# Optimization experiments

Hardware: AMD Instinct MI355X
Metric: run time of the kernel (lower is better)

Reference implementation:

```python
import jax, jax.numpy as jnp
import numpy as np

N_HEADS = 16

def setup_inputs() -> dict:
    key = jax.random.key(0)
    ks = jax.random.split(key, 8)
    B, S, D = 2, 2048, 1024
    s = 0.02
    return {
        "hidden_states": jax.random.normal(ks[0], (B, S, D), jnp.float32),
        "attention_mask": jnp.ones((B, S), jnp.int32),
        "script_types": jax.random.randint(ks[1], (B, S), 0, 4),
        "Wq": jax.random.normal(ks[2], (D, D), jnp.float32) * s,
        "bq": jnp.zeros((D,), jnp.float32),
        "Wk": jax.random.normal(ks[3], (D, D), jnp.float32) * s,
        "bk": jnp.zeros((D,), jnp.float32),
        "Wv": jax.random.normal(ks[4], (D, D), jnp.float32) * s,
        "bv": jnp.zeros((D,), jnp.float32),
        "Wo": jax.random.normal(ks[5], (D, D), jnp.float32) * s,
        "bo": jnp.zeros((D,), jnp.float32),
        "script_w": jnp.ones((4, N_HEADS), jnp.float32),
    }

def _heads(x, H):
    B, S, D = x.shape
    return x.reshape(B, S, H, D // H).transpose(0, 2, 1, 3)  # [B,H,S,hd]

def reference(hidden_states, attention_mask, script_types, Wq, bq, Wk, bk, Wv, bv, Wo, bo, script_w):
    B, S, D = hidden_states.shape
    H = N_HEADS
    hd = D // H
    q = _heads(hidden_states @ Wq + bq, H)
    k = _heads(hidden_states @ Wk + bk, H)
    v = _heads(hidden_states @ Wv + bv, H)
    # script-dependent per-head query scaling: [B,S,H] -> [B,H,S,1]
    sw = script_w[script_types].transpose(0, 2, 1)[..., None]
    q = q * sw
    scores = jnp.einsum("bhqd,bhkd->bhqk", q, k) / jnp.sqrt(jnp.float32(hd))
    mask = attention_mask[:, None, None, :]  # [B,1,1,S]
    scores = jnp.where(mask == 0, -jnp.inf, scores)
    probs = jax.nn.softmax(scores, axis=-1)  # dropout is identity in eval mode
    ctx = jnp.einsum("bhqk,bhkd->bhqd", probs, v)
    ctx = ctx.transpose(0, 2, 1, 3).reshape(B, S, D)
    out = ctx @ Wo + bo
    return out, probs
```

## Files before the change

kernel.cpp:

```cpp
#include <hip/hip_runtime.h>
#include <hip/hip_bf16.h>
#include <cstdint>
#include <cstddef>

typedef __attribute__((ext_vector_type(8))) short short8;
typedef __attribute__((ext_vector_type(4))) float f32x4;

#define MFMA16(a,b,c) __builtin_amdgcn_mfma_f32_16x16x32_bf16((a),(b),(c),0,0,0)
#define NEG_INF (-__builtin_inff())

__device__ __forceinline__ unsigned short f2bf(float f) {
    union { float f; unsigned int u; } a; a.f = f;
    return (unsigned short)((a.u + 0x7FFFu + ((a.u >> 16) & 1u)) >> 16);
}

__device__ __forceinline__ void gload16(const void* g, void* l) {
    __builtin_amdgcn_global_load_lds(
        (const __attribute__((address_space(1))) void*)g,
        (__attribute__((address_space(3))) void*)l, 16, 0, 0);
}

__global__ __launch_bounds__(256) void prep(const float* __restrict__ X,
                                            unsigned short* __restrict__ Xb,
                                            const float* __restrict__ Wq,
                                            const float* __restrict__ Wk,
                                            const float* __restrict__ Wv,
                                            const float* __restrict__ Wo,
                                            unsigned short* __restrict__ WqkvT,
                                            unsigned short* __restrict__ WoT,
                                            const float* __restrict__ bq,
                                            const float* __restrict__ bk,
                                            const float* __restrict__ bv,
                                            float* __restrict__ biasq) {
    const int bid = blockIdx.x;
    const int t = threadIdx.x;
    if (bid < 4096) {
        int i = (bid * 256 + t) * 4;
        float4 v = *(const float4*)(X + i);
        ushort4 o;
        o.x = f2bf(v.x); o.y = f2bf(v.y); o.z = f2bf(v.z); o.w = f2bf(v.w);
        *(ushort4*)(Xb + i) = o;
    } else if (bid < 8192) {
        __shared__ float tile[32][33];
        const int wid = bid - 4096;
        const int which = wid >> 10, t32 = wid & 1023;
        const float* W = (which == 0) ? Wq : (which == 1) ? Wk : (which == 2) ? Wv : Wo;
        unsigned short* WT = (which < 3) ? (WqkvT + which * 1048576) : WoT;
        int tx = t & 31, ty = t >> 5;
        int kb = (t32 & 31) * 32, nb = (t32 >> 5) * 32;
        #pragma unroll
        for (int r = 0; r < 32; r += 8)
            tile[ty + r][tx] = W[(size_t)(kb + ty + r) * 1024 + nb + tx];
        __syncthreads();
        #pragma unroll
        for (int r = 0; r < 32; r += 8) {
            float v = tile[tx][ty + r];
            WT[(size_t)(nb + ty + r) * 1024 + kb + tx] = f2bf(v);
        }
    } else {
        for (int i = t; i < 3072; i += 256) {
            const float* s = (i < 1024) ? bq : (i < 2048) ? bk : bv;
            biasq[i] = s[i & 1023];
        }
    }
}

__global__ __launch_bounds__(256) void gemm_qkv(const unsigned short* __restrict__ A,
                                                const unsigned short* __restrict__ BT,
                                                const float* __restrict__ bias,
                                                unsigned short* __restrict__ qk_out,
                                                unsigned short* __restrict__ vt_out) {
    __shared__ alignas(16) unsigned short As[4096];
    __shared__ alignas(16) unsigned short Bs[4096];
    const int t = threadIdx.x;
    const int wave = t >> 6, lane = t & 63, quad = lane >> 4, l16 = lane & 15;
    const int m0 = blockIdx.x * 128, n0 = blockIdx.y * 128;
    const int wm = (wave >> 1) * 64, wn = (wave & 1) * 64;
    const int r4 = lane >> 2, c16 = (lane & 3) << 4;
    const char* Ag = (const char*)A + (size_t)(m0 + wave * 32 + r4) * 2048 + c16;
    const char* Bg = (const char*)BT + (size_t)(n0 + wave * 32 + r4) * 2048 + c16;
    char* Al = (char*)As + wave * 2048;
    char* Bl = (char*)Bs + wave * 2048;
    f32x4 acc[4][4] = {};
    for (int k0 = 0; k0 < 1024; k0 += 32) {
        __syncthreads();
        gload16(Ag + k0 * 2, Al);
        gload16(Ag + k0 * 2 + 32768, Al + 1024);
        gload16(Bg + k0 * 2, Bl);
        gload16(Bg + k0 * 2 + 32768, Bl + 1024);
        __syncthreads();
        short8 af[4], bfr[4];
        #pragma unroll
        for (int i = 0; i < 4; i++)
            af[i] = *(const short8*)((const char*)As + (wm + i * 16 + l16) * 64 + (quad << 4));
        #pragma unroll
        for (int j = 0; j < 4; j++)
            bfr[j] = *(const short8*)((const char*)Bs + (wn + j * 16 + l16) * 64 + (quad << 4));
        #pragma unroll
        for (int i = 0; i < 4; i++)
            #pragma unroll
            for (int j = 0; j < 4; j++)
                acc[i][j] = MFMA16(af[i], bfr[j], acc[i][j]);
    }
    #pragma unroll
    for (int i = 0; i < 4; i++) {
        int tokb = m0 + wm + i * 16 + quad * 4;
        int b = tokb >> 11, s = tokb & 2047;
        #pragma unroll
        for (int j = 0; j < 4; j++) {
            int n = n0 + wn + j * 16 + l16;
            float bv = bias[n];
            int which = n >> 10, n1 = n & 1023, h = n1 >> 6, d = n1 & 63;
            if (which == 2) {
                ushort4 pv;
                pv.x = f2bf(acc[i][j][0] + bv);
                pv.y = f2bf(acc[i][j][1] + bv);
                pv.z = f2bf(acc[i][j][2] + bv);
                pv.w = f2bf(acc[i][j][3] + bv);
                *(ushort4*)(vt_out + ((size_t)(b * 16 + h) * 64 + d) * 2048 + s) = pv;
            } else {
                #pragma unroll
                for (int r = 0; r < 4; r++) {
                    float v = acc[i][j][r] + bv;
                    qk_out[(size_t)which * 4194304 +
                           (((size_t)(b * 16 + h)) * 2048 + s + r) * 64 + d] = f2bf(v);
                }
            }
        }
    }
}

__global__ __launch_bounds__(256) void gemm_out(const unsigned short* __restrict__ A,
                                                const unsigned short* __restrict__ BT,
                                                const float* __restrict__ bias,
                                                float* __restrict__ C) {
    __shared__ alignas(16) unsigned short As[2048];
    __shared__ alignas(16) unsigned short Bs[4096];
    const int t = threadIdx.x;
    const int wave = t >> 6, lane = t & 63, quad = lane >> 4, l16 = lane & 15;
    const int m0 = blockIdx.x * 64, n0 = blockIdx.y * 128;
    const int wm = (wave >> 1) * 32, wn = (wave & 1) * 64;
    const int r4 = lane >> 2, c16 = (lane & 3) << 4;
    const char* Ag = (const char*)A + (size_t)(m0 + wave * 16 + r4) * 2048 + c16;
    const char* Bg = (const char*)BT + (size_t)(n0 + wave * 32 + r4) * 2048 + c16;
    char* Al = (char*)As + wave * 1024;
    char* Bl = (char*)Bs + wave * 2048;
    f32x4 acc[2][4] = {};
    for (int k0 = 0; k0 < 1024; k0 += 32) {
        __syncthreads();
        gload16(Ag + k0 * 2, Al);
        gload16(Bg + k0 * 2, Bl);
        gload16(Bg + k0 * 2 + 32768, Bl + 1024);
        __syncthreads();
        short8 af[2], bfr[4];
        #pragma unroll
        for (int i = 0; i < 2; i++)
            af[i] = *(const short8*)((const char*)As + (wm + i * 16 + l16) * 64 + (quad << 4));
        #pragma unroll
        for (int j = 0; j < 4; j++)
            bfr[j] = *(const short8*)((const char*)Bs + (wn + j * 16 + l16) * 64 + (quad << 4));
        #pragma unroll
        for (int i = 0; i < 2; i++)
            #pragma unroll
            for (int j = 0; j < 4; j++)
                acc[i][j] = MFMA16(af[i], bfr[j], acc[i][j]);
    }
    #pragma unroll
    for (int i = 0; i < 2; i++) {
        int tokb = m0 + wm + i * 16 + quad * 4;
        #pragma unroll
        for (int j = 0; j < 4; j++) {
            int n = n0 + wn + j * 16 + l16;
            float bv = bias[n];
            #pragma unroll
            for (int r = 0; r < 4; r++)
                C[(size_t)(tokb + r) * 1024 + n] = acc[i][j][r] + bv;
        }
    }
}

__global__ __launch_bounds__(512, 4) void attn(const unsigned short* __restrict__ Q,
                                               const unsigned short* __restrict__ K,
                                               const unsigned short* __restrict__ Vt,
                                               const int* __restrict__ amask,
                                               const int* __restrict__ stypes,
                                               const float* __restrict__ script_w,
                                               float* __restrict__ probs,
                                               unsigned short* __restrict__ ctx) {
    __shared__ alignas(16) unsigned short Ks[2][4096];
    __shared__ alignas(16) unsigned short Vts[2][4096];
    __shared__ alignas(16) unsigned short Ps[8][16][64];
    const int t = threadIdx.x;
    const int wave = t >> 6, lane = t & 63, quad = lane >> 4, l16 = lane & 15;
    const int bid = blockIdx.y * 16 + blockIdx.x;
    const int swz = (bid & 7) * 64 + (bid >> 3);
    const int qt = swz & 15, bh = swz >> 4;
    const int b = bh >> 4, h = bh & 15;
    const int q0 = qt * 128;
    const int qrow = q0 + wave * 16 + l16;
    const int sx16 = (l16 & 7) << 4;

    const int st = stypes[b * 2048 + qrow];
    const float sfac = script_w[st * 16 + h] * 0.125f;

    const size_t qbase = ((size_t)bh * 2048 + qrow) * 64;
    const short8 aQ0 = *(const short8*)(Q + qbase + quad * 8);
    const short8 aQ1 = *(const short8*)(Q + qbase + 32 + quad * 8);

    const char* Kg = (const char*)(K + (size_t)bh * 131072);
    const char* Vg = (const char*)(Vt + (size_t)bh * 131072);
    const int* am = amask + b * 2048;

    const int r8 = lane >> 3;
    const int cx = ((lane & 7) ^ r8) << 4;

#define STAGE_K(kt_, buf_) \
    gload16(Kg + (size_t)(kt_) * 8192 + (wave * 8 + r8) * 128 + cx, \
            (char*)&Ks[buf_][0] + wave * 1024)
#define STAGE_V(kt_, buf_) \
    gload16(Vg + (size_t)(wave * 8 + r8) * 4096 + (kt_) * 128 + cx, \
            (char*)&Vts[buf_][0] + wave * 1024)

    float lsum = 0.f;
    STAGE_K(0, 0);
    __syncthreads();
    {
        int cur = 0;
        for (int kt = 0; kt < 32; kt++) {
            if (kt < 31) STAGE_K(kt + 1, cur ^ 1);
            __builtin_amdgcn_sched_barrier(0);
            f32x4 sc[4] = {};
            const char* kbl = (const char*)&Ks[cur][0];
            __builtin_amdgcn_s_setprio(1);
            #pragma unroll
            for (int j = 0; j < 4; j++) {
                const char* rp = kbl + (j * 16 + l16) * 128;
                short8 bk0 = *(const short8*)(rp + ((quad << 4) ^ sx16));
                short8 bk1 = *(const short8*)(rp + ((64 + (quad << 4)) ^ sx16));
                sc[j] = MFMA16(bk0, aQ0, sc[j]);
                sc[j] = MFMA16(bk1, aQ1, sc[j]);
            }
            __builtin_amdgcn_s_setprio(0);
            #pragma unroll
            for (int j = 0; j < 4; j++) {
                int4 mi = *(const int4*)(am + kt * 64 + j * 16 + quad * 4);
                lsum += __expf(fmaf(sc[j][0], sfac, mi.x ? 0.f : NEG_INF));
                lsum += __expf(fmaf(sc[j][1], sfac, mi.y ? 0.f : NEG_INF));
                lsum += __expf(fmaf(sc[j][2], sfac, mi.z ? 0.f : NEG_INF));
                lsum += __expf(fmaf(sc[j][3], sfac, mi.w ? 0.f : NEG_INF));
            }
            __syncthreads();
            cur ^= 1;
        }
    }
    lsum += __shfl_xor(lsum, 16, 64);
    lsum += __shfl_xor(lsum, 32, 64);
    const float lbias = (lsum > 0.f) ? -__logf(lsum) : NEG_INF;

    f32x4 oacc[4] = {};
    STAGE_K(0, 0);
    STAGE_V(0, 0);
    asm volatile("s_waitcnt vmcnt(0)" ::: "memory");
    __builtin_amdgcn_s_barrier();
    __builtin_amdgcn_sched_barrier(0);
    {
        int cur = 0;
        char* psrow = (char*)&Ps[wave][l16][0];
        for (int kt = 0; kt < 32; kt++) {
            if (kt < 31) { STAGE_K(kt + 1, cur ^ 1); STAGE_V(kt + 1, cur ^ 1); }
            __builtin_amdgcn_sched_barrier(0);
            f32x4 sc[4] = {};
            const char* kbl = (const char*)&Ks[cur][0];
            __builtin_amdgcn_s_setprio(1);
            #pragma unroll
            for (int j = 0; j < 4; j++) {
                const char* rp = kbl + (j * 16 + l16) * 128;
                short8 bk0 = *(const short8*)(rp + ((quad << 4) ^ sx16));
                short8 bk1 = *(const short8*)(rp + ((64 + (quad << 4)) ^ sx16));
                sc[j] = MFMA16(bk0, aQ0, sc[j]);
                sc[j] = MFMA16(bk1, aQ1, sc[j]);
            }
            __builtin_amdgcn_s_setprio(0);
            short8 v0[4], v1[4];
            const char* vbl = (const char*)&Vts[cur][0];
            #pragma unroll
            for (int j2 = 0; j2 < 4; j2++) {
                const char* rp = vbl + (j2 * 16 + l16) * 128;
                v0[j2] = *(const short8*)(rp + ((quad << 4) ^ sx16));
                v1[j2] = *(const short8*)(rp + ((64 + (quad << 4)) ^ sx16));
            }
            const size_t pbase = ((size_t)bh * 2048 + qrow) * 2048 + kt * 64 + quad * 4;
            #pragma unroll
            for (int j = 0; j < 4; j++) {
                int4 mi = *(const int4*)(am + kt * 64 + j * 16 + quad * 4);
                float p0 = __expf(fmaf(sc[j][0], sfac, mi.x ? lbias : NEG_INF));
                float p1 = __expf(fmaf(sc[j][1], sfac, mi.y ? lbias : NEG_INF));
                float p2 = __expf(fmaf(sc[j][2], sfac, mi.z ? lbias : NEG_INF));
                float p3 = __expf(fmaf(sc[j][3], sfac, mi.w ? lbias : NEG_INF));
                f32x4 pv; pv[0] = p0; pv[1] = p1; pv[2] = p2; pv[3] = p3;
                __builtin_nontemporal_store(pv, (f32x4*)(probs + pbase + j * 16));
                ushort4 pq; pq.x = f2bf(p0); pq.y = f2bf(p1); pq.z = f2bf(p2); pq.w = f2bf(p3);
                *(ushort4*)(psrow + ((j * 32 + quad * 8) ^ sx16)) = pq;
            }
            asm volatile("s_waitcnt lgkmcnt(0)" ::: "memory");
            __builtin_amdgcn_sched_barrier(0);
            short8 aP0 = *(const short8*)(psrow + ((quad << 4) ^ sx16));
            short8 aP1 = *(const short8*)(psrow + ((64 + (quad << 4)) ^ sx16));
            __builtin_amdgcn_s_setprio(1);
            #pragma unroll
            for (int j2 = 0; j2 < 4; j2++) oacc[j2] = MFMA16(aP0, v0[j2], oacc[j2]);
            #pragma unroll
            for (int j2 = 0; j2 < 4; j2++) oacc[j2] = MFMA16(aP1, v1[j2], oacc[j2]);
            __builtin_amdgcn_s_setprio(0);
            asm volatile("s_waitcnt vmcnt(4)" ::: "memory");
            __builtin_amdgcn_s_barrier();
            __builtin_amdgcn_sched_barrier(0);
            cur ^= 1;
        }
    }
#undef STAGE_K
#undef STAGE_V
    #pragma unroll
    for (int j2 = 0; j2 < 4; j2++)
        #pragma unroll
        for (int r = 0; r < 4; r++) {
            int qr = q0 + wave * 16 + quad * 4 + r;
            ctx[((size_t)b * 2048 + qr) * 1024 + h * 64 + j2 * 16 + l16] = f2bf(oacc[j2][r]);
        }
}

extern "C" void kernel_launch(void* const* d_in, const int* in_sizes, int n_in,
                              void* d_out, int out_size, void* d_ws, size_t ws_size,
                              hipStream_t stream) {
    const float* X    = (const float*)d_in[0];
    const int*  amask = (const int*)d_in[1];
    const int*  stp   = (const int*)d_in[2];
    const float* Wq   = (const float*)d_in[3];
    const float* bq   = (const float*)d_in[4];
    const float* Wk   = (const float*)d_in[5];
    const float* bk   = (const float*)d_in[6];
    const float* Wv   = (const float*)d_in[7];
    const float* bv   = (const float*)d_in[8];
    const float* Wo   = (const float*)d_in[9];
    const float* bo   = (const float*)d_in[10];
    const float* sw   = (const float*)d_in[11];

    float* out   = (float*)d_out;
    float* probs = out + 4194304;

    char* ws = (char*)d_ws;
    unsigned short* Xb    = (unsigned short*)(ws);
    unsigned short* WqkvT = (unsigned short*)(ws + 8388608);
    unsigned short* WoT   = (unsigned short*)(ws + 14680064);
    float*          biasq = (float*)(ws + 16777216);
    unsigned short* Qb    = (unsigned short*)(ws + 16789504);
    unsigned short* Vtb   = (unsigned short*)(ws + 41955328);
    unsigned short* Ctx   = (unsigned short*)(ws + 50343936);
    unsigned short* Kb    = Qb + 4194304;

    prep<<<8193, 256, 0, stream>>>(X, Xb, Wq, Wk, Wv, Wo, WqkvT, WoT, bq, bk, bv, biasq);
    gemm_qkv<<<dim3(32, 24), 256, 0, stream>>>(Xb, WqkvT, biasq, Qb, Vtb);
    attn<<<dim3(16, 32), 512, 0, stream>>>(Qb, Kb, Vtb, amask, stp, sw, probs, Ctx);
    gemm_out<<<dim3(64, 8), 256, 0, stream>>>(Ctx, WoT, bo, out);
}
```

Baseline: 296.7 us.

## Triple-buffer K/V tiles and software-pipeline QK^T of the next tile in attention

Expands the K and V LDS staging from double to triple buffers, prefetching two tiles ahead. It also computes the next tile's QK^T scores while the current tile's softmax and PV work runs, to overlap MFMA with the exp and store work. The attention mask is converted once into an additive float bias in LDS. The softmax now multiplies by a reciprocal sum instead of adding a log bias, and uses packed v_cvt_pk_bf16 conversion. V fragments are loaded in two halves to cut register pressure. The larger LDS footprint (about 72KB per block) may reduce the number of resident blocks per CU, and vmcnt(4) now also waits on the two-ahead prefetch.

```diff
diff --git a/kernel.cpp b/kernel.cpp
--- a/kernel.cpp
+++ b/kernel.cpp
@@ -12,6 +12,12 @@
 __device__ __forceinline__ unsigned short f2bf(float f) {
     union { float f; unsigned int u; } a; a.f = f;
     return (unsigned short)((a.u + 0x7FFFu + ((a.u >> 16) & 1u)) >> 16);
+}
+
+__device__ __forceinline__ unsigned int cvtpk_bf16(float a, float b) {
+    unsigned int r;
+    asm("v_cvt_pk_bf16_f32 %0, %1, %2" : "=v"(r) : "v"(a), "v"(b));
+    return r;
 }
 
 __device__ __forceinline__ void gload16(const void* g, void* l) {
@@ -187,9 +193,10 @@
                                                const float* __restrict__ script_w,
                                                float* __restrict__ probs,
                                                unsigned short* __restrict__ ctx) {
-    __shared__ alignas(16) unsigned short Ks[2][4096];
-    __shared__ alignas(16) unsigned short Vts[2][4096];
+    __shared__ alignas(16) unsigned short KsA[3][4096];
+    __shared__ alignas(16) unsigned short VtsA[3][4096];
     __shared__ alignas(16) unsigned short Ps[8][16][64];
+    __shared__ alignas(16) float mb[2048];
     const int t = threadIdx.x;
     const int wave = t >> 6, lane = t & 63, quad = lane >> 4, l16 = lane & 15;
     const int bid = blockIdx.y * 16 + blockIdx.x;
@@ -209,117 +216,121 @@
 
     const char* Kg = (const char*)(K + (size_t)bh * 131072);
     const char* Vg = (const char*)(Vt + (size_t)bh * 131072);
-    const int* am = amask + b * 2048;
+
+    {
+        int4 m4 = *(const int4*)(amask + b * 2048 + t * 4);
+        f32x4 mv;
+        mv[0] = m4.x ? 0.f : NEG_INF;
+        mv[1] = m4.y ? 0.f : NEG_INF;
+        mv[2] = m4.z ? 0.f : NEG_INF;
+        mv[3] = m4.w ? 0.f : NEG_INF;
+        *(f32x4*)&mb[t * 4] = mv;
+    }
 
     const int r8 = lane >> 3;
     const int cx = ((lane & 7) ^ r8) << 4;
-
-#define STAGE_K(kt_, buf_) \
-    gload16(Kg + (size_t)(kt_) * 8192 + (wave * 8 + r8) * 128 + cx, \
-            (char*)&Ks[buf_][0] + wave * 1024)
-#define STAGE_V(kt_, buf_) \
-    gload16(Vg + (size_t)(wave * 8 + r8) * 4096 + (kt_) * 128 + cx, \
-            (char*)&Vts[buf_][0] + wave * 1024)
+    char* KsB = (char*)&KsA[0][0];
+    char* VtsB = (char*)&VtsA[0][0];
+
+#define STAGE_K(kt_, ob_) \
+    gload16(Kg + (size_t)(kt_) * 8192 + (wave * 8 + r8) * 128 + cx, KsB + (ob_) + wave * 1024)
+#define STAGE_V(kt_, ob_) \
+    gload16(Vg + (size_t)(wave * 8 + r8) * 4096 + (kt_) * 128 + cx, VtsB + (ob_) + wave * 1024)
+#define QKT(dst_, ob_) do { \
+        const char* _kb = KsB + (ob_); \
+        _Pragma("unroll") \
+        for (int _j = 0; _j < 4; _j++) { \
+            const char* _rp = _kb + (_j * 16 + l16) * 128; \
+            short8 _k0 = *(const short8*)(_rp + ((quad << 4) ^ sx16)); \
+            short8 _k1 = *(const short8*)(_rp + ((64 + (quad << 4)) ^ sx16)); \
+            dst_[_j] = MFMA16(_k0, aQ0, dst_[_j]); \
+            dst_[_j] = MFMA16(_k1, aQ1, dst_[_j]); \
+        } } while (0)
+
+    int ob0 = 0, ob1 = 8192, ob2 = 16384;
 
     float lsum = 0.f;
-    STAGE_K(0, 0);
+    STAGE_K(0, ob0);
+    STAGE_K(1, ob1);
     __syncthreads();
-    {
-        int cur = 0;
-        for (int kt = 0; kt < 32; kt++) {
-            if (kt < 31) STAGE_K(kt + 1, cur ^ 1);
-            __builtin_amdgcn_sched_barrier(0);
-            f32x4 sc[4] = {};
-            const char* kbl = (const char*)&Ks[cur][0];
-            __builtin_amdgcn_s_setprio(1);
-            #pragma unroll
-            for (int j = 0; j < 4; j++) {
-                const char* rp = kbl + (j * 16 + l16) * 128;
-                short8 bk0 = *(const short8*)(rp + ((quad << 4) ^ sx16));
-                short8 bk1 = *(const short8*)(rp + ((64 + (quad << 4)) ^ sx16));
-                sc[j] = MFMA16(bk0, aQ0, sc[j]);
-                sc[j] = MFMA16(bk1, aQ1, sc[j]);
-            }
-            __builtin_amdgcn_s_setprio(0);
-            #pragma unroll
-            for (int j = 0; j < 4; j++) {
-                int4 mi = *(const int4*)(am + kt * 64 + j * 16 + quad * 4);
-                lsum += __expf(fmaf(sc[j][0], sfac, mi.x ? 0.f : NEG_INF));
-                lsum += __expf(fmaf(sc[j][1], sfac, mi.y ? 0.f : NEG_INF));
-                lsum += __expf(fmaf(sc[j][2], sfac, mi.z ? 0.f : NEG_INF));
-                lsum += __expf(fmaf(sc[j][3], sfac, mi.w ? 0.f : NEG_INF));
-            }
-            __syncthreads();
-            cur ^= 1;
-        }
+    f32x4 sc[4] = {};
+    QKT(sc, ob0);
+    for (int kt = 0; kt < 32; kt++) {
+        if (kt < 30) STAGE_K(kt + 2, ob2);
+        #pragma unroll
+        for (int j = 0; j < 4; j++) {
+            f32x4 mv = *(const f32x4*)&mb[kt * 64 + j * 16 + quad * 4];
+            float e0 = __expf(fmaf(sc[j][0], sfac, mv[0]));
+            float e1 = __expf(fmaf(sc[j][1], sfac, mv[1]));
+            float e2 = __expf(fmaf(sc[j][2], sfac, mv[2]));
+            float e3 = __expf(fmaf(sc[j][3], sfac, mv[3]));
+            lsum += (e0 + e1) + (e2 + e3);
+        }
+        f32x4 scn[4] = {};
+        if (kt < 31) QKT(scn, ob1);
+        __syncthreads();
+        int tmp = ob0; ob0 = ob1; ob1 = ob2; ob2 = tmp;
+        #pragma unroll
+        for (int j = 0; j < 4; j++) sc[j] = scn[j];
     }
     lsum += __shfl_xor(lsum, 16, 64);
     lsum += __shfl_xor(lsum, 32, 64);
-    const float lbias = (lsum > 0.f) ? -__logf(lsum) : NEG_INF;
+    const float inv_l = (lsum > 0.f) ? 1.0f / lsum : 0.0f;
 
     f32x4 oacc[4] = {};
-    STAGE_K(0, 0);
-    STAGE_V(0, 0);
-    asm volatile("s_waitcnt vmcnt(0)" ::: "memory");
-    __builtin_amdgcn_s_barrier();
-    __builtin_amdgcn_sched_barrier(0);
-    {
-        int cur = 0;
-        char* psrow = (char*)&Ps[wave][l16][0];
-        for (int kt = 0; kt < 32; kt++) {
-            if (kt < 31) { STAGE_K(kt + 1, cur ^ 1); STAGE_V(kt + 1, cur ^ 1); }
-            __builtin_amdgcn_sched_barrier(0);
-            f32x4 sc[4] = {};
-            const char* kbl = (const char*)&Ks[cur][0];
-            __builtin_amdgcn_s_setprio(1);
-            #pragma unroll
-            for (int j = 0; j < 4; j++) {
-                const char* rp = kbl + (j * 16 + l16) * 128;
-                short8 bk0 = *(const short8*)(rp + ((quad << 4) ^ sx16));
-                short8 bk1 = *(const short8*)(rp + ((64 + (quad << 4)) ^ sx16));
-                sc[j] = MFMA16(bk0, aQ0, sc[j]);
-                sc[j] = MFMA16(bk1, aQ1, sc[j]);
-            }
-            __builtin_amdgcn_s_setprio(0);
-            short8 v0[4], v1[4];
-            const char* vbl = (const char*)&Vts[cur][0];
-            #pragma unroll
-            for (int j2 = 0; j2 < 4; j2++) {
-                const char* rp = vbl + (j2 * 16 + l16) * 128;
-                v0[j2] = *(const short8*)(rp + ((quad << 4) ^ sx16));
-                v1[j2] = *(const short8*)(rp + ((64 + (quad << 4)) ^ sx16));
-            }
-            const size_t pbase = ((size_t)bh * 2048 + qrow) * 2048 + kt * 64 + quad * 4;
-            #pragma unroll
-            for (int j = 0; j < 4; j++) {
-                int4 mi = *(const int4*)(am + kt * 64 + j * 16 + quad * 4);
-                float p0 = __expf(fmaf(sc[j][0], sfac, mi.x ? lbias : NEG_INF));
-                float p1 = __expf(fmaf(sc[j][1], sfac, mi.y ? lbias : NEG_INF));
-                float p2 = __expf(fmaf(sc[j][2], sfac, mi.z ? lbias : NEG_INF));
-                float p3 = __expf(fmaf(sc[j][3], sfac, mi.w ? lbias : NEG_INF));
-                f32x4 pv; pv[0] = p0; pv[1] = p1; pv[2] = p2; pv[3] = p3;
-                __builtin_nontemporal_store(pv, (f32x4*)(probs + pbase + j * 16));
-                ushort4 pq; pq.x = f2bf(p0); pq.y = f2bf(p1); pq.z = f2bf(p2); pq.w = f2bf(p3);
-                *(ushort4*)(psrow + ((j * 32 + quad * 8) ^ sx16)) = pq;
-            }
-            asm volatile("s_waitcnt lgkmcnt(0)" ::: "memory");
-            __builtin_amdgcn_sched_barrier(0);
-            short8 aP0 = *(const short8*)(psrow + ((quad << 4) ^ sx16));
-            short8 aP1 = *(const short8*)(psrow + ((64 + (quad << 4)) ^ sx16));
-            __builtin_amdgcn_s_setprio(1);
-            #pragma unroll
-            for (int j2 = 0; j2 < 4; j2++) oacc[j2] = MFMA16(aP0, v0[j2], oacc[j2]);
-            #pragma unroll
-            for (int j2 = 0; j2 < 4; j2++) oacc[j2] = MFMA16(aP1, v1[j2], oacc[j2]);
-            __builtin_amdgcn_s_setprio(0);
-            asm volatile("s_waitcnt vmcnt(4)" ::: "memory");
-            __builtin_amdgcn_s_barrier();
-            __builtin_amdgcn_sched_barrier(0);
-            cur ^= 1;
-        }
+    ob0 = 0; ob1 = 8192; ob2 = 16384;
+    STAGE_K(0, ob0); STAGE_V(0, ob0);
+    STAGE_K(1, ob1); STAGE_V(1, ob1);
+    __syncthreads();
+    f32x4 sc2[4] = {};
+    QKT(sc2, ob0);
+    char* psrow = (char*)&Ps[wave][l16][0];
+    for (int kt = 0; kt < 32; kt++) {
+        if (kt < 30) { STAGE_K(kt + 2, ob2); STAGE_V(kt + 2, ob2); }
+        const size_t pbase = ((size_t)bh * 2048 + qrow) * 2048 + kt * 64 + quad * 4;
+        #pragma unroll
+        for (int j = 0; j < 4; j++) {
+            f32x4 mv = *(const f32x4*)&mb[kt * 64 + j * 16 + quad * 4];
+            float p0 = __expf(fmaf(sc2[j][0], sfac, mv[0])) * inv_l;
+            float p1 = __expf(fmaf(sc2[j][1], sfac, mv[1])) * inv_l;
+            float p2 = __expf(fmaf(sc2[j][2], sfac, mv[2])) * inv_l;
+            float p3 = __expf(fmaf(sc2[j][3], sfac, mv[3])) * inv_l;
+            f32x4 pv; pv[0] = p0; pv[1] = p1; pv[2] = p2; pv[3] = p3;
+            __builtin_nontemporal_store(pv, (f32x4*)(probs + pbase + j * 16));
+            uint2 pq; pq.x = cvtpk_bf16(p0, p1); pq.y = cvtpk_bf16(p2, p3);
+            *(uint2*)(psrow + ((j * 32 + quad * 8) ^ sx16)) = pq;
+        }
+        const char* vbl = VtsB + ob0;
+        short8 vv[4];
+        #pragma unroll
+        for (int j2 = 0; j2 < 4; j2++)
+            vv[j2] = *(const short8*)(vbl + (j2 * 16 + l16) * 128 + ((quad << 4) ^ sx16));
+        f32x4 scn[4] = {};
+        if (kt < 31) QKT(scn, ob1);
+        asm volatile("s_waitcnt lgkmcnt(0)" ::: "memory");
+        __builtin_amdgcn_sched_barrier(0);
+        short8 aP0 = *(const short8*)(psrow + ((quad << 4) ^ sx16));
+        short8 aP1 = *(const short8*)(psrow + ((64 + (quad << 4)) ^ sx16));
+        __builtin_amdgcn_s_setprio(1);
+        #pragma unroll
+        for (int j2 = 0; j2 < 4; j2++) oacc[j2] = MFMA16(aP0, vv[j2], oacc[j2]);
+        __builtin_amdgcn_s_setprio(0);
+        #pragma unroll
+        for (int j2 = 0; j2 < 4; j2++)
+            vv[j2] = *(const short8*)(vbl + (j2 * 16 + l16) * 128 + ((64 + (quad << 4)) ^ sx16));
+        __builtin_amdgcn_s_setprio(1);
+        #pragma unroll
+        for (int j2 = 0; j2 < 4; j2++) oacc[j2] = MFMA16(aP1, vv[j2], oacc[j2]);
+        __builtin_amdgcn_s_setprio(0);
+        asm volatile("s_waitcnt vmcnt(4)" ::: "memory");
+        __builtin_amdgcn_s_barrier();
+        int tmp = ob0; ob0 = ob1; ob1 = ob2; ob2 = tmp;
+        #pragma unroll
+        for (int j = 0; j < 4; j++) sc2[j] = scn[j];
     }
 #undef STAGE_K
 #undef STAGE_V
+#undef QKT
     #pragma unroll
     for (int j2 = 0; j2 < 4; j2++)
         #pragma unroll
```

Measured after the change: 288.2 us. -2.9%, faster.
